# Kernel optimization log

Measured on AMD Instinct MI355X. Metric: run time of the kernel, lower is better.

The kernel has to match this reference:

```python
import jax, jax.numpy as jnp
import numpy as np

# Dims: batch, seq, model dim, heads, routes-per-query, bleed-over alpha
B, S, D, H, K_ROUTES = 4, 512, 1024, 16, 64
HD = D // H                      # head_dim = 64
SCALE = 1.0 / float(np.sqrt(HD))
ALPHA = 0.25                     # neighbor bleed-over (forward arg default 0.0; >0 here)
CAUSAL = True
NEG = jnp.float32(-1e9)


def _build_routes(seq_len: int, k: int, depth: int = 8) -> np.ndarray:
    """Cantor-coordinate based positional routes (mirrors _build_positional_routes)."""
    pos = np.arange(seq_len, dtype=np.float64)
    x = pos / max(1, seq_len - 1)
    x = np.clip(x, 1e-6, 1.0 - 1e-6)
    val = np.zeros_like(x)
    factor = 0.5
    for _ in range(depth):
        xs = x * 3.0
        digit = xs.astype(np.int64)
        frac = xs - digit
        val = val + (digit == 2).astype(np.float64) * factor
        x = frac
        factor *= 0.5
    coords = np.clip(val, 0.0, 1.0)
    dist = np.abs(coords[:, None] - coords[None, :])            # [S,S]
    routes = np.argsort(dist, axis=1, kind='stable')[:, :k]     # k smallest distances
    return routes.astype(np.int32)


def setup_inputs() -> dict:
    key = jax.random.key(0)
    k0, k1, k2 = jax.random.split(key, 3)
    x = jax.random.normal(k0, (B, S, D), dtype=jnp.float32)
    # nn.Linear weights stored pre-transposed as [in, out] for clean matmul
    w_qkv = jax.random.normal(k1, (D, 3 * D), dtype=jnp.float32) * (1.0 / np.sqrt(D))
    b_qkv = jnp.zeros((3 * D,), dtype=jnp.float32)
    w_out = jax.random.normal(k2, (D, D), dtype=jnp.float32) * (1.0 / np.sqrt(D))
    b_out = jnp.zeros((D,), dtype=jnp.float32)
    routes = jnp.asarray(_build_routes(S, K_ROUTES), dtype=jnp.int32)  # [S, K]
    return {"x": x, "w_qkv": w_qkv, "b_qkv": b_qkv,
            "w_out": w_out, "b_out": b_out, "routes": routes}


def reference(x, w_qkv, b_qkv, w_out, b_out, routes):
    # QKV projection: [B,S,3D] -> [3,B,H,S,hd]
    qkv = (x @ w_qkv + b_qkv).reshape(B, S, 3, H, HD).transpose(2, 0, 3, 1, 4)
    q, k, v = qkv[0], qkv[1], qkv[2]                 # each [B,H,S,hd]

    r = routes                                        # [S,K]
    k_g = jnp.take(k, r, axis=2)                      # [B,H,S,K,hd]
    v_g = jnp.take(v, r, axis=2)
    if ALPHA > 0.0:
        rl = jnp.clip(r - 1, 0, S - 1)
        rr = jnp.clip(r + 1, 0, S - 1)
        k_g = (1.0 - ALPHA) * k_g + (ALPHA / 2.0) * (jnp.take(k, rl, axis=2) + jnp.take(k, rr, axis=2))
        v_g = (1.0 - ALPHA) * v_g + (ALPHA / 2.0) * (jnp.take(v, rl, axis=2) + jnp.take(v, rr, axis=2))

    scores = jnp.einsum('bhqd,bhqkd->bhqk', q, k_g) * SCALE   # [B,H,S,K]
    if CAUSAL:
        # route index > query position is masked (each query always routes to itself)
        mask = r > jnp.arange(S, dtype=r.dtype)[:, None]       # [S,K]
        scores = jnp.where(mask[None, None], NEG, scores)

    attn = jax.nn.softmax(scores, axis=-1)
    out = jnp.einsum('bhqk,bhqkd->bhqd', attn, v_g)            # [B,H,S,hd]
    out = out.transpose(0, 2, 1, 3).reshape(B, S, D)
    return out @ w_out + b_out
```

## Files before the change

kernel.cpp:

```cpp
#include <hip/hip_runtime.h>
#include <hip/hip_bf16.h>

#define BB 4
#define SS 512
#define DD 1024
#define HH 16
#define KR 64
#define HDIM 64
#define THREE_D 3072
#define M_ROWS 2048
#define SCALE_F 0.125f

typedef __attribute__((ext_vector_type(8))) short short8;
typedef __attribute__((ext_vector_type(4))) float floatx4;

union F8 { short8 s; unsigned int u[4]; unsigned short h[8]; };

__device__ inline float bfu(unsigned short h){ union{unsigned int u; float f;} c; c.u = ((unsigned int)h) << 16; return c.f; }
__device__ inline unsigned short f2bf(float f){
    union{float f; unsigned int u;} c; c.f = f;
    unsigned int u = c.u;
    return (unsigned short)((u + 0x7fffu + ((u >> 16) & 1u)) >> 16);
}

#define GLOAD_LDS16(g, l)                                                     \
    __builtin_amdgcn_global_load_lds(                                         \
        (const __attribute__((address_space(1))) unsigned int*)(g),           \
        (__attribute__((address_space(3))) unsigned int*)(l), 16, 0, 0)

__global__ __launch_bounds__(256) void prep_kernel(
    const float* __restrict__ x, const float* __restrict__ w_qkv,
    const float* __restrict__ w_out, const int* __restrict__ routes,
    unsigned short* __restrict__ xb_sw, unsigned short* __restrict__ wb1_sw,
    unsigned short* __restrict__ wb2_sw, unsigned int* __restrict__ maskg)
{
    const int bx = blockIdx.x;
    const int tid = threadIdx.x;
    if (bx < 1024) {
        int gid = bx * 256 + tid;
        int r  = gid & 127;
        int c  = (gid >> 7) & 3;
        int kt = (gid >> 9) & 31;
        int mt = gid >> 14;
        const float* src = x + ((size_t)(mt * 128 + r)) * 1024 + kt * 32 + c * 8;
        float4 a = *(const float4*)src;
        float4 b = *(const float4*)(src + 4);
        F8 o;
        o.h[0] = f2bf(a.x); o.h[1] = f2bf(a.y); o.h[2] = f2bf(a.z); o.h[3] = f2bf(a.w);
        o.h[4] = f2bf(b.x); o.h[5] = f2bf(b.y); o.h[6] = f2bf(b.z); o.h[7] = f2bf(b.w);
        *(uint4*)(xb_sw + (size_t)gid * 8) = *(uint4*)&o;
    } else if (bx < 3072) {
        const float* w;
        unsigned short* out;
        int gid, N;
        if (bx < 2560) { w = w_qkv; out = wb1_sw; N = THREE_D; gid = (bx - 1024) * 256 + tid; }
        else           { w = w_out; out = wb2_sw; N = DD;      gid = (bx - 2560) * 256 + tid; }
        int r  = gid & 127;
        int c  = (gid >> 7) & 3;
        int kt = (gid >> 9) & 31;
        int nt = gid >> 14;
        int n = nt * 128 + r;
        int kbase = kt * 32 + c * 8;
        F8 o;
#pragma unroll
        for (int j = 0; j < 8; ++j)
            o.h[j] = f2bf(w[(size_t)(kbase + j) * N + n]);
        *(uint4*)(out + (size_t)gid * 8) = *(uint4*)&o;
    } else {
        int q = (bx - 3072) * 256 + tid;
        unsigned int w[16];
#pragma unroll
        for (int i = 0; i < 16; ++i) w[i] = 0u;
        for (int j = 0; j < KR; ++j) {
            int r = routes[q * KR + j];
            if (r <= q) w[r >> 5] |= 1u << (r & 31);
        }
#pragma unroll
        for (int sw = 0; sw < 16; ++sw) maskg[sw * SS + q] = w[sw];
    }
}

__global__ __launch_bounds__(256) void gemm_qkv(
    const unsigned short* __restrict__ Asw,
    const unsigned short* __restrict__ Bsw,
    const float* __restrict__ bias,
    unsigned short* __restrict__ qb, unsigned short* __restrict__ kb,
    unsigned short* __restrict__ vb)
{
    __shared__ __align__(16) unsigned short Sh[12288];
    unsigned short* Alds = Sh;
    unsigned short* Blds = Sh + 4096;

    const int tid  = threadIdx.x;
    const int lane = tid & 63;
    const int wid  = tid >> 6;
    const int l15  = lane & 15;
    const int quad = lane >> 4;

    const int bid  = blockIdx.x;
    const int xcd  = bid & 7;
    const int loc  = bid >> 3;
    const int mt64 = (xcd & 3) * 8 + (loc & 7);
    const int nt   = (xcd >> 2) * 12 + (loc >> 3);

    const int mt = mt64 >> 1;
    const int rh = (mt64 & 1) * 64;
    const int wn = wid * 32;

    floatx4 acc[4][2];
#pragma unroll
    for (int i = 0; i < 4; ++i)
#pragma unroll
        for (int j = 0; j < 2; ++j) acc[i][j] = (floatx4){0.f, 0.f, 0.f, 0.f};

    for (int kt2 = 0; kt2 < 16; ++kt2) {
#pragma unroll
        for (int kh = 0; kh < 2; ++kh) {
            int kt = kt2 * 2 + kh;
            const unsigned short* ga = Asw + ((size_t)(mt * 32 + kt) * 4 + wid) * 1024 + (rh + lane) * 8;
            const unsigned short* gb = Bsw + (size_t)(nt * 32 + kt) * 4096 + wid * 1024 + lane * 8;
            GLOAD_LDS16(ga,       Alds + kh * 2048 + wid * 512 + lane * 8);
            GLOAD_LDS16(gb,       Blds + kh * 4096 + wid * 1024 + lane * 8);
            GLOAD_LDS16(gb + 512, Blds + kh * 4096 + wid * 1024 + 512 + lane * 8);
        }
        __syncthreads();

#pragma unroll
        for (int kh = 0; kh < 2; ++kh) {
            F8 af[4], bf[2];
#pragma unroll
            for (int mi = 0; mi < 4; ++mi)
                af[mi] = *(const F8*)(Alds + kh * 2048 + (size_t)(quad * 64 + mi * 16 + l15) * 8);
#pragma unroll
            for (int ni = 0; ni < 2; ++ni)
                bf[ni] = *(const F8*)(Blds + kh * 4096 + (size_t)(quad * 128 + wn + ni * 16 + l15) * 8);
#pragma unroll
            for (int mi = 0; mi < 4; ++mi)
#pragma unroll
                for (int ni = 0; ni < 2; ++ni)
                    acc[mi][ni] = __builtin_amdgcn_mfma_f32_16x16x32_bf16(
                        af[mi].s, bf[ni].s, acc[mi][ni], 0, 0, 0);
        }
        __syncthreads();
    }

    const int m0 = mt64 * 64;
    const int n0 = nt * 128;

#pragma unroll
    for (int mi = 0; mi < 4; ++mi) {
#pragma unroll
        for (int ni = 0; ni < 2; ++ni) {
            int col = wn + ni * 16 + l15;
            float bv = bias[n0 + col];
#pragma unroll
            for (int r = 0; r < 4; ++r) {
                int row = mi * 16 + quad * 4 + r;
                Sh[row * 136 + col] = f2bf(acc[mi][ni][r] + bv);
            }
        }
    }
    __syncthreads();

    for (int i = tid; i < 1024; i += 256) {
        int rr = i >> 4, cc = i & 15;
        int grow = m0 + rr, gcol = n0 + cc * 8;
        int b = grow >> 9, s = grow & 511;
        int which = gcol >> 10, rem = gcol & 1023;
        int h = rem >> 6, hd = rem & 63;
        unsigned short* dst = (which == 0) ? qb : (which == 1) ? kb : vb;
        uint4 val = *(const uint4*)(Sh + rr * 136 + cc * 8);
        *(uint4*)(dst + (((size_t)(b * HH + h) * SS) + s) * HDIM + hd) = val;
    }
}

__global__ __launch_bounds__(256) void gemm_out(
    const unsigned short* __restrict__ Asw,
    const unsigned short* __restrict__ Bsw,
    const float* __restrict__ bias,
    float* __restrict__ Cout)
{
    __shared__ __align__(16) unsigned short Alds[4096];
    __shared__ __align__(16) unsigned short Blds[4096];

    const int tid  = threadIdx.x;
    const int lane = tid & 63;
    const int wid  = tid >> 6;
    const int l15  = lane & 15;
    const int quad = lane >> 4;

    const int bid  = blockIdx.x;
    const int xcd  = bid & 7;
    const int loc  = bid >> 3;
    const int mt64 = (xcd & 3) * 8 + (loc & 7);
    const int nt64 = (xcd >> 2) * 8 + (loc >> 3);

    const int mt  = mt64 >> 1;
    const int rh  = (mt64 & 1) * 64;
    const int ntB = nt64 >> 1;
    const int rhB = (nt64 & 1) * 64;
    const int wm  = (wid >> 1) * 32;
    const int wn  = (wid & 1) * 32;

    floatx4 acc[2][2];
#pragma unroll
    for (int i = 0; i < 2; ++i)
#pragma unroll
        for (int j = 0; j < 2; ++j) acc[i][j] = (floatx4){0.f, 0.f, 0.f, 0.f};

    for (int kt2 = 0; kt2 < 16; ++kt2) {
#pragma unroll
        for (int kh = 0; kh < 2; ++kh) {
            int kt = kt2 * 2 + kh;
            const unsigned short* ga = Asw + ((size_t)(mt  * 32 + kt) * 4 + wid) * 1024 + (rh  + lane) * 8;
            const unsigned short* gb = Bsw + ((size_t)(ntB * 32 + kt) * 4 + wid) * 1024 + (rhB + lane) * 8;
            GLOAD_LDS16(ga, Alds + kh * 2048 + wid * 512 + lane * 8);
            GLOAD_LDS16(gb, Blds + kh * 2048 + wid * 512 + lane * 8);
        }
        __syncthreads();

#pragma unroll
        for (int kh = 0; kh < 2; ++kh) {
            F8 af[2], bf[2];
#pragma unroll
            for (int mi = 0; mi < 2; ++mi)
                af[mi] = *(const F8*)(Alds + kh * 2048 + (size_t)(quad * 64 + wm + mi * 16 + l15) * 8);
#pragma unroll
            for (int ni = 0; ni < 2; ++ni)
                bf[ni] = *(const F8*)(Blds + kh * 2048 + (size_t)(quad * 64 + wn + ni * 16 + l15) * 8);
#pragma unroll
            for (int mi = 0; mi < 2; ++mi)
#pragma unroll
                for (int ni = 0; ni < 2; ++ni)
                    acc[mi][ni] = __builtin_amdgcn_mfma_f32_16x16x32_bf16(
                        af[mi].s, bf[ni].s, acc[mi][ni], 0, 0, 0);
        }
        __syncthreads();
    }

    const int m0 = mt64 * 64;
    const int n0 = nt64 * 64;
#pragma unroll
    for (int mi = 0; mi < 2; ++mi) {
#pragma unroll
        for (int ni = 0; ni < 2; ++ni) {
            int col = n0 + wn + ni * 16 + l15;
            float bv = bias[col];
#pragma unroll
            for (int r = 0; r < 4; ++r) {
                int row = m0 + wm + mi * 16 + quad * 4 + r;
                Cout[(size_t)row * DD + col] = acc[mi][ni][r] + bv;
            }
        }
    }
}

__global__ __launch_bounds__(256) void blend_kv_kernel(
    const unsigned short* __restrict__ kb, const unsigned short* __restrict__ vb,
    unsigned short* __restrict__ K2g, unsigned short* __restrict__ Vtg)
{
    __shared__ float vt[130][65];
    const int bh = blockIdx.x >> 2;
    const int qd = blockIdx.x & 3;
    const int s0 = qd * 128;
    const int tid = threadIdx.x;
    const unsigned short* kbase = kb + (size_t)bh * SS * HDIM;
    const unsigned short* vbase = vb + (size_t)bh * SS * HDIM;
    unsigned short* Kq = K2g + ((size_t)(bh * 4 + qd)) * 8192;
    unsigned short* Vq = Vtg + ((size_t)(bh * 4 + qd)) * 8192;

    for (int i = tid; i < 130 * 8; i += 256) {
        int row = i >> 3, c8 = (i & 7) << 3;
        int s = s0 + row - 1; s = s < 0 ? 0 : (s > SS - 1 ? SS - 1 : s);
        F8 vv = *(const F8*)(vbase + (size_t)s * 64 + c8);
#pragma unroll
        for (int j = 0; j < 8; ++j) vt[row][c8 + j] = bfu(vv.h[j]);
    }

    for (int i = tid; i < 1024; i += 256) {
        int sl = i >> 3, cc = i & 7;
        int s = s0 + sl;
        int sm = s ? s - 1 : 0;
        int sp = (s < SS - 1) ? s + 1 : SS - 1;
        F8 k0 = *(const F8*)(kbase + (size_t)s  * 64 + cc * 8);
        F8 km = *(const F8*)(kbase + (size_t)sm * 64 + cc * 8);
        F8 kp = *(const F8*)(kbase + (size_t)sp * 64 + cc * 8);
        F8 o;
#pragma unroll
        for (int j = 0; j < 8; ++j)
            o.h[j] = f2bf(0.75f * bfu(k0.h[j]) + 0.125f * (bfu(km.h[j]) + bfu(kp.h[j])));
        *(uint4*)(Kq + (size_t)(sl * 8 + (cc ^ (sl & 7))) * 8) = *(uint4*)&o;
    }
    __syncthreads();

    for (int i = tid; i < 1024; i += 256) {
        int d = i >> 4, scl = i & 15;
        F8 o;
#pragma unroll
        for (int a = 0; a < 8; ++a) {
            int rl = scl * 8 + a;
            o.h[a] = f2bf(0.75f * vt[rl + 1][d] + 0.125f * (vt[rl][d] + vt[rl + 2][d]));
        }
        int chunk = d * 16 + (scl & 8) + ((scl ^ d) & 7);
        *(uint4*)(Vq + (size_t)chunk * 8) = *(uint4*)&o;
    }
}

__global__ __launch_bounds__(512) void attn_kernel(
    const unsigned short* __restrict__ qb,
    const unsigned short* __restrict__ K2g,
    const unsigned short* __restrict__ Vtg,
    const unsigned int* __restrict__ maskg,
    unsigned short* __restrict__ attn_sw)
{
    __shared__ __align__(16) unsigned short Ks2[2][8192];
    __shared__ __align__(16) unsigned short Vs2[2][8192];
    __shared__ __align__(16) unsigned short Ps[8192];

    const int bh = blockIdx.x >> 2;
    const int qt = blockIdx.x & 3;
    const int b = bh >> 4, h = bh & 15;
    const int tid  = threadIdx.x;
    const int lane = tid & 63;
    const int wid  = tid >> 6;
    const int l15  = lane & 15;
    const int quad = lane >> 4;

    const unsigned short* Kbh = K2g + (size_t)bh * 4 * 8192;
    const unsigned short* Vbh = Vtg + (size_t)bh * 4 * 8192;

    #define STAGE(qd, bufi) do {                                              \
        const unsigned short* kq = Kbh + (size_t)(qd) * 8192;                 \
        const unsigned short* vq = Vbh + (size_t)(qd) * 8192;                 \
        GLOAD_LDS16(kq + wid * 1024 + lane * 8,       Ks2[bufi] + wid * 1024 + lane * 8);        \
        GLOAD_LDS16(kq + wid * 1024 + 512 + lane * 8, Ks2[bufi] + wid * 1024 + 512 + lane * 8);  \
        GLOAD_LDS16(vq + wid * 1024 + lane * 8,       Vs2[bufi] + wid * 1024 + lane * 8);        \
        GLOAD_LDS16(vq + wid * 1024 + 512 + lane * 8, Vs2[bufi] + wid * 1024 + 512 + lane * 8);  \
    } while (0)

    const int qbase = qt * 128 + wid * 16;
    const int q = qbase + l15;

    F8 qf[2];
    {
        const unsigned short* qrow = qb + ((size_t)bh * SS + q) * 64;
        qf[0] = *(const F8*)(qrow + quad * 8);
        qf[1] = *(const F8*)(qrow + 32 + quad * 8);
    }

    STAGE(0, 0);
    __syncthreads();

    floatx4 accO[4];
#pragma unroll
    for (int dt = 0; dt < 4; ++dt) accO[dt] = (floatx4){0.f, 0.f, 0.f, 0.f};
    float lsum = 0.f;
    unsigned int* Pw = (unsigned int*)Ps + wid * 512;

    for (int qd = 0; qd < 4; ++qd) {
        if (qd < 3) STAGE(qd + 1, (qd + 1) & 1);
        const unsigned short* Ksb = Ks2[qd & 1];
        const unsigned short* Vsb = Vs2[qd & 1];

        floatx4 accS[8];
#pragma unroll
        for (int st = 0; st < 8; ++st) {
            int srow = st * 16 + l15;
            const F8 k0 = *(const F8*)(Ksb + (((srow << 3) | ( quad      ^ (srow & 7))) << 3));
            const F8 k1 = *(const F8*)(Ksb + (((srow << 3) | ((4 + quad) ^ (srow & 7))) << 3));
            floatx4 a = (floatx4){0.f, 0.f, 0.f, 0.f};
            a = __builtin_amdgcn_mfma_f32_16x16x32_bf16(k0.s, qf[0].s, a, 0, 0, 0);
            a = __builtin_amdgcn_mfma_f32_16x16x32_bf16(k1.s, qf[1].s, a, 0, 0, 0);
            accS[st] = a;
        }

#pragma unroll
        for (int ch2 = 0; ch2 < 2; ++ch2) {
            unsigned int mw0 = maskg[(qd * 4 + ch2 * 2) * SS + q];
            unsigned int mw1 = maskg[(qd * 4 + ch2 * 2 + 1) * SS + q];
#pragma unroll
            for (int t = 0; t < 4; ++t) {
                unsigned int mw = (t & 2) ? mw1 : mw0;
                int sbase = (t & 1) * 16 + quad * 4;
                floatx4 a = accS[ch2 * 4 + t];
                float e0 = ((mw >> (sbase + 0)) & 1u) ? __expf(a[0] * SCALE_F) : 0.f;
                float e1 = ((mw >> (sbase + 1)) & 1u) ? __expf(a[1] * SCALE_F) : 0.f;
                float e2 = ((mw >> (sbase + 2)) & 1u) ? __expf(a[2] * SCALE_F) : 0.f;
                float e3 = ((mw >> (sbase + 3)) & 1u) ? __expf(a[3] * SCALE_F) : 0.f;
                lsum += (e0 + e1) + (e2 + e3);
                unsigned int w0 = (unsigned int)f2bf(e0) | ((unsigned int)f2bf(e1) << 16);
                unsigned int w1 = (unsigned int)f2bf(e2) | ((unsigned int)f2bf(e3) << 16);
                int off0 = t * 8 + quad * 2;
                int off1 = off0 + 1;
                Pw[l15 * 32 + ((((off0 >> 2) ^ (l15 & 7)) << 2) | (off0 & 3))] = w0;
                Pw[l15 * 32 + ((((off1 >> 2) ^ (l15 & 7)) << 2) | (off1 & 3))] = w1;
            }
            F8 pa[2];
#pragma unroll
            for (int ks = 0; ks < 2; ++ks) {
                int ci = ks * 4 + quad;
                pa[ks] = *(const F8*)((const unsigned short*)(Pw + l15 * 32) +
                                      ((ci ^ (l15 & 7)) << 3));
            }
#pragma unroll
            for (int dt = 0; dt < 4; ++dt) {
                int d = dt * 16 + l15;
#pragma unroll
                for (int ks = 0; ks < 2; ++ks) {
                    int scl = ch2 * 8 + ks * 4 + quad;
                    int chunk = d * 16 + (scl & 8) + ((scl ^ d) & 7);
                    const F8 bv = *(const F8*)(Vsb + ((size_t)chunk << 3));
                    accO[dt] = __builtin_amdgcn_mfma_f32_16x16x32_bf16(pa[ks].s, bv.s, accO[dt], 0, 0, 0);
                }
            }
        }
        __syncthreads();
    }

    lsum += __shfl_xor(lsum, 16);
    lsum += __shfl_xor(lsum, 32);
    float inv = 1.0f / lsum;

    unsigned short* Ow = Ps + wid * 1024;
#pragma unroll
    for (int r = 0; r < 4; ++r) {
        float invr = __shfl(inv, quad * 4 + r);
#pragma unroll
        for (int dt = 0; dt < 4; ++dt)
            Ow[(quad * 4 + r) * 64 + dt * 16 + l15] = f2bf(accO[dt][r] * invr);
    }
#pragma unroll
    for (int i = 0; i < 2; ++i) {
        int ch = i * 64 + lane;
        int qlocal = ch >> 3, j = ch & 7;
        int qq = qt * 128 + wid * 16 + qlocal;
        int mrow = b * SS + qq;
        int mt = mrow >> 7, rr = mrow & 127;
        int kt2 = h * 2 + (j >> 2), c = j & 3;
        size_t gid = (((size_t)(mt * 32 + kt2) * 4 + c) * 128 + rr);
        *(uint4*)(attn_sw + gid * 8) = *(const uint4*)(Ow + qlocal * 64 + j * 8);
    }
    #undef STAGE
}

extern "C" void kernel_launch(void* const* d_in, const int* in_sizes, int n_in,
                              void* d_out, int out_size, void* d_ws, size_t ws_size,
                              hipStream_t stream)
{
    const float* x     = (const float*)d_in[0];
    const float* w_qkv = (const float*)d_in[1];
    const float* b_qkv = (const float*)d_in[2];
    const float* w_out = (const float*)d_in[3];
    const float* b_out = (const float*)d_in[4];
    const int* routes  = (const int*)d_in[5];

    char* w = (char*)d_ws;
    unsigned short* xb_sw  = (unsigned short*)(w);
    unsigned short* wb1_sw = (unsigned short*)(w + (4u  << 20));
    unsigned short* wb2_sw = (unsigned short*)(w + (10u << 20));
    unsigned short* qbuf   = (unsigned short*)(w + (12u << 20));
    unsigned short* kbuf   = (unsigned short*)(w + (16u << 20));
    unsigned short* vbuf   = (unsigned short*)(w + (20u << 20));
    unsigned short* K2g    = (unsigned short*)(w + (24u << 20));
    unsigned short* Vtg    = (unsigned short*)(w + (28u << 20));
    unsigned short* attnsw = (unsigned short*)(w + (32u << 20));
    unsigned int*   maskg  = (unsigned int*)(w + (36u << 20));

    prep_kernel<<<3074, 256, 0, stream>>>(x, w_qkv, w_out, routes,
                                          xb_sw, wb1_sw, wb2_sw, maskg);

    gemm_qkv<<<768, 256, 0, stream>>>(xb_sw, wb1_sw, b_qkv, qbuf, kbuf, vbuf);

    blend_kv_kernel<<<256, 256, 0, stream>>>(kbuf, vbuf, K2g, Vtg);

    attn_kernel<<<256, 512, 0, stream>>>(qbuf, K2g, Vtg, maskg, attnsw);

    gemm_out<<<512, 256, 0, stream>>>(attnsw, wb2_sw, b_out, (float*)d_out);
}
```

Baseline: 145.4 us.

## Deepen QKV GEMM k-staging and split attention into smaller XCD-mapped blocks

The QKV GEMM now stages four k-tiles per barrier instead of two, doubling its LDS buffer, so there are half as many __syncthreads per output tile. The attention kernel moves from 256 blocks of 512 threads to 512 blocks of 256 threads, each covering 64 queries. Block ids are remapped so that blocks sharing a batch-head land on the same XCD, and each wave stages more K/V chunks. The aim is better occupancy, more blocks in flight and better L2 locality, at the cost of loading each head's K/V twice as often and more LDS in the GEMM.

```diff
diff --git a/kernel.cpp b/kernel.cpp
--- a/kernel.cpp
+++ b/kernel.cpp
@@ -87,9 +87,9 @@
     unsigned short* __restrict__ qb, unsigned short* __restrict__ kb,
     unsigned short* __restrict__ vb)
 {
-    __shared__ __align__(16) unsigned short Sh[12288];
+    __shared__ __align__(16) unsigned short Sh[24576];
     unsigned short* Alds = Sh;
-    unsigned short* Blds = Sh + 4096;
+    unsigned short* Blds = Sh + 8192;
 
     const int tid  = threadIdx.x;
     const int lane = tid & 63;
@@ -113,10 +113,10 @@
 #pragma unroll
         for (int j = 0; j < 2; ++j) acc[i][j] = (floatx4){0.f, 0.f, 0.f, 0.f};
 
-    for (int kt2 = 0; kt2 < 16; ++kt2) {
-#pragma unroll
-        for (int kh = 0; kh < 2; ++kh) {
-            int kt = kt2 * 2 + kh;
+    for (int kt8 = 0; kt8 < 8; ++kt8) {
+#pragma unroll
+        for (int kh = 0; kh < 4; ++kh) {
+            int kt = kt8 * 4 + kh;
             const unsigned short* ga = Asw + ((size_t)(mt * 32 + kt) * 4 + wid) * 1024 + (rh + lane) * 8;
             const unsigned short* gb = Bsw + (size_t)(nt * 32 + kt) * 4096 + wid * 1024 + lane * 8;
             GLOAD_LDS16(ga,       Alds + kh * 2048 + wid * 512 + lane * 8);
@@ -126,7 +126,7 @@
         __syncthreads();
 
 #pragma unroll
-        for (int kh = 0; kh < 2; ++kh) {
+        for (int kh = 0; kh < 4; ++kh) {
             F8 af[4], bf[2];
 #pragma unroll
             for (int mi = 0; mi < 4; ++mi)
@@ -306,7 +306,7 @@
     }
 }
 
-__global__ __launch_bounds__(512) void attn_kernel(
+__global__ __launch_bounds__(256) void attn_kernel(
     const unsigned short* __restrict__ qb,
     const unsigned short* __restrict__ K2g,
     const unsigned short* __restrict__ Vtg,
@@ -315,10 +315,13 @@
 {
     __shared__ __align__(16) unsigned short Ks2[2][8192];
     __shared__ __align__(16) unsigned short Vs2[2][8192];
-    __shared__ __align__(16) unsigned short Ps[8192];
-
-    const int bh = blockIdx.x >> 2;
-    const int qt = blockIdx.x & 3;
+    __shared__ __align__(16) unsigned short Ps[4096];
+
+    const int bid = blockIdx.x;
+    const int xcd = bid & 7;
+    const int loc = bid >> 3;
+    const int bh  = xcd * 8 + (loc & 7);
+    const int qt  = loc >> 3;
     const int b = bh >> 4, h = bh & 15;
     const int tid  = threadIdx.x;
     const int lane = tid & 63;
@@ -330,16 +333,21 @@
     const unsigned short* Vbh = Vtg + (size_t)bh * 4 * 8192;
 
     #define STAGE(qd, bufi) do {                                              \
-        const unsigned short* kq = Kbh + (size_t)(qd) * 8192;                 \
-        const unsigned short* vq = Vbh + (size_t)(qd) * 8192;                 \
-        GLOAD_LDS16(kq + wid * 1024 + lane * 8,       Ks2[bufi] + wid * 1024 + lane * 8);        \
-        GLOAD_LDS16(kq + wid * 1024 + 512 + lane * 8, Ks2[bufi] + wid * 1024 + 512 + lane * 8);  \
-        GLOAD_LDS16(vq + wid * 1024 + lane * 8,       Vs2[bufi] + wid * 1024 + lane * 8);        \
-        GLOAD_LDS16(vq + wid * 1024 + 512 + lane * 8, Vs2[bufi] + wid * 1024 + 512 + lane * 8);  \
+        const unsigned short* kq = Kbh + (size_t)(qd) * 8192 + wid * 2048;    \
+        const unsigned short* vq = Vbh + (size_t)(qd) * 8192 + wid * 2048;    \
+        unsigned short* kl = Ks2[bufi] + wid * 2048;                          \
+        unsigned short* vl = Vs2[bufi] + wid * 2048;                          \
+        GLOAD_LDS16(kq + lane * 8,        kl + lane * 8);                     \
+        GLOAD_LDS16(kq + 512 + lane * 8,  kl + 512 + lane * 8);               \
+        GLOAD_LDS16(kq + 1024 + lane * 8, kl + 1024 + lane * 8);              \
+        GLOAD_LDS16(kq + 1536 + lane * 8, kl + 1536 + lane * 8);              \
+        GLOAD_LDS16(vq + lane * 8,        vl + lane * 8);                     \
+        GLOAD_LDS16(vq + 512 + lane * 8,  vl + 512 + lane * 8);               \
+        GLOAD_LDS16(vq + 1024 + lane * 8, vl + 1024 + lane * 8);              \
+        GLOAD_LDS16(vq + 1536 + lane * 8, vl + 1536 + lane * 8);              \
     } while (0)
 
-    const int qbase = qt * 128 + wid * 16;
-    const int q = qbase + l15;
+    const int q = qt * 64 + wid * 16 + l15;
 
     F8 qf[2];
     {
@@ -433,7 +441,7 @@
     for (int i = 0; i < 2; ++i) {
         int ch = i * 64 + lane;
         int qlocal = ch >> 3, j = ch & 7;
-        int qq = qt * 128 + wid * 16 + qlocal;
+        int qq = qt * 64 + wid * 16 + qlocal;
         int mrow = b * SS + qq;
         int mt = mrow >> 7, rr = mrow & 127;
         int kt2 = h * 2 + (j >> 2), c = j & 3;
@@ -473,7 +481,7 @@
 
     blend_kv_kernel<<<256, 256, 0, stream>>>(kbuf, vbuf, K2g, Vtg);
 
-    attn_kernel<<<256, 512, 0, stream>>>(qbuf, K2g, Vtg, maskg, attnsw);
+    attn_kernel<<<512, 256, 0, stream>>>(qbuf, K2g, Vtg, maskg, attnsw);
 
     gemm_out<<<512, 256, 0, stream>>>(attnsw, wb2_sw, b_out, (float*)d_out);
 }
```

Measured after the change: 144.5 us. About the same (-0.6%).
